# Optimization experiments

Hardware: AMD Instinct MI355X
Metric: run time of the kernel (lower is better)

Reference implementation:

```python
import jax, jax.numpy as jnp
import numpy as np

N_NODES, N_EDGES, NUM_GRAPHS = 50000, 800000, 64
F_DIM, H_DIM, N_LAYERS, N_CLASSES = 64, 64, 3, 16
EPS = 1e-5  # StdAggregation epsilon (PyG)


def setup_inputs() -> dict:
    key = jax.random.key(0)
    ks = jax.random.split(key, 12)
    s = 0.05
    x = jax.random.normal(ks[0], (N_NODES, F_DIM), jnp.float32)
    edge_index = jax.random.randint(ks[1], (2, N_EDGES), 0, N_NODES, dtype=jnp.int32)
    batch = jnp.sort(jax.random.randint(ks[2], (N_NODES,), 0, NUM_GRAPHS, dtype=jnp.int32))
    # per-layer PNAConv params (towers=1): pre Linear(2F->F), post Linear(13F->H), lin Linear(H->H)
    pre_w = jax.random.normal(ks[3], (N_LAYERS, F_DIM, 2 * F_DIM), jnp.float32) * s
    pre_b = jnp.zeros((N_LAYERS, F_DIM), jnp.float32)
    post_w = jax.random.normal(ks[4], (N_LAYERS, H_DIM, 13 * F_DIM), jnp.float32) * s
    post_b = jnp.zeros((N_LAYERS, H_DIM), jnp.float32)
    lin_w = jax.random.normal(ks[5], (N_LAYERS, H_DIM, H_DIM), jnp.float32) * s
    lin_b = jnp.zeros((N_LAYERS, H_DIM), jnp.float32)
    mlp_w1 = jax.random.normal(ks[6], (H_DIM, H_DIM), jnp.float32) * s
    mlp_b1 = jnp.zeros((H_DIM,), jnp.float32)
    mlp_w2 = jax.random.normal(ks[7], (N_CLASSES, H_DIM), jnp.float32) * s
    mlp_b2 = jnp.zeros((N_CLASSES,), jnp.float32)
    return dict(x=x, edge_index=edge_index, batch=batch,
                pre_w=pre_w, pre_b=pre_b, post_w=post_w, post_b=post_b,
                lin_w=lin_w, lin_b=lin_b, mlp_w1=mlp_w1, mlp_b1=mlp_b1,
                mlp_w2=mlp_w2, mlp_b2=mlp_b2)


def pna_forward(x, src, dst, pre_w, pre_b, post_w, post_b, lin_w, lin_b,
                mlp_w1, mlp_b1, mlp_w2, mlp_b2, batch):
    N = x.shape[0]
    deg_raw = jax.ops.segment_sum(jnp.ones_like(src, jnp.float32), dst, N)  # in-degree [N]
    deg = jnp.maximum(deg_raw, 1.0)[:, None]
    # avg log degree (PNA avg_deg['log'] from the degree histogram of this graph)
    avg_log = jnp.mean(jnp.log(deg_raw + 1.0))
    log_deg = jnp.log(deg + 1.0)
    amp = log_deg / avg_log          # amplification scaler [N,1]
    att = avg_log / log_deg          # attenuation scaler [N,1]
    has_in = (deg_raw > 0)[:, None]

    for l in range(pre_w.shape[0]):
        h = jnp.concatenate([x[dst], x[src]], axis=-1)        # [E, 2F] (x_i, x_j)
        m = h @ pre_w[l].T + pre_b[l]                          # pre_nn message [E, F]
        s1 = jax.ops.segment_sum(m, dst, N)
        s2 = jax.ops.segment_sum(m * m, dst, N)
        mean = s1 / deg
        std = jnp.sqrt(jax.nn.relu(s2 / deg - mean * mean) + EPS)
        mn = jnp.where(has_in, jax.ops.segment_min(m, dst, N), 0.0)
        mx = jnp.where(has_in, jax.ops.segment_max(m, dst, N), 0.0)
        aggr = jnp.concatenate([mean, mn, mx, std], axis=-1)   # [N, 4F]
        out = jnp.concatenate([x, aggr, aggr * amp, aggr * att], axis=-1)  # [N, 13F]
        out = out @ post_w[l].T + post_b[l]                    # post_nn [N, H]
        x = jax.nn.relu(out @ lin_w[l].T + lin_b[l])           # conv.lin + outer ReLU

    # global mean pool over graphs
    counts = jnp.maximum(
        jax.ops.segment_sum(jnp.ones((N,), x.dtype), batch, NUM_GRAPHS), 1.0)
    g = jax.ops.segment_sum(x, batch, NUM_GRAPHS) / counts[:, None]  # [G, H]
    g = jax.nn.relu(g @ mlp_w1.T + mlp_b1)
    return g @ mlp_w2.T + mlp_b2                               # [G, C]


def reference(x, edge_index, batch, pre_w, pre_b, post_w, post_b,
              lin_w, lin_b, mlp_w1, mlp_b1, mlp_w2, mlp_b2):
    src, dst = edge_index[0], edge_index[1]
    return pna_forward(x, src, dst, pre_w, pre_b, post_w, post_b,
                       lin_w, lin_b, mlp_w1, mlp_b1, mlp_w2, mlp_b2, batch)
```

## Files before the change

### kernel.cpp

```cpp
#include <hip/hip_runtime.h>
#include <math.h>

#define N_NODES   50000
#define N_EDGES   800000
#define NUM_GRAPHS 64
#define FDIM      64
#define HDIM      64
#define NLAYERS   3
#define NCLASSES  16
#define EPS       1e-5f

#define SCAN_CHUNK 1024
#define NCHUNKS ((N_NODES + SCAN_CHUNK - 1) / SCAN_CHUNK)

typedef unsigned short u16;
typedef unsigned int   u32;
typedef __attribute__((ext_vector_type(8))) short short8;
typedef __attribute__((ext_vector_type(4))) float floatx4;

#define WKS_LAYER 159744
#define PRES_LAYER 24576

__device__ inline void split1(float f, u16& h, u16& m, u16& l) {
    u32 b  = __float_as_uint(f);
    u32 hb = b & 0xFFFF0000u;
    float r = f - __uint_as_float(hb);
    u32 mb = __float_as_uint(r) & 0xFFFF0000u;
    float r2 = r - __uint_as_float(mb);
    u32 lb = __float_as_uint(r2) & 0xFFFF0000u;
    h = (u16)(hb >> 16); m = (u16)(mb >> 16); l = (u16)(lb >> 16);
}

__device__ inline void gl_lds16(const void* g, void* l) {
    __builtin_amdgcn_global_load_lds(
        (const __attribute__((address_space(1))) u32*)g,
        (__attribute__((address_space(3))) u32*)l, 16, 0, 0);
}

__global__ __launch_bounds__(256) void k_comb(const float* __restrict__ post_w,
                                              const float* __restrict__ lin_w,
                                              const float* __restrict__ pre_w,
                                              const float* __restrict__ post_b,
                                              const float* __restrict__ lin_b,
                                              u16* __restrict__ WkS,
                                              u16* __restrict__ PreS,
                                              float* __restrict__ bcv,
                                              int* __restrict__ cnt,
                                              float* __restrict__ logsum) {
    int b = blockIdx.x, t = threadIdx.x;
    int zi = b * 256 + t;
    if (zi < N_NODES) cnt[zi] = 0;
    if (zi == 0) *logsum = 0.f;

    if (b < 624) {
        int c  = t & 63;
        int kl = t >> 6;
        int l  = b / 208;
        int o  = (b % 208) * 4 + kl;
        const float* lw = lin_w + (size_t)l * 4096 + c * 64;
        const float* pw = post_w + (size_t)l * 53248 + o;
        float acc = 0.f;
        #pragma unroll 8
        for (int j = 0; j < 64; ++j)
            acc += lw[j] * pw[(size_t)j * 832];
        u16 h, m, lo;
        split1(acc, h, m, lo);

        int kn;
        if (o < 64) kn = o;
        else {
            int s  = (o - 64) >> 8;
            int mm = (o - 64) & 255;
            int j  = mm >> 5, r = mm & 31;
            kn = 64 + j * 96 + s * 32 + r;
        }
        int ch  = kn >> 5;
        int kin = kn & 31;
        int n16 = c & 15, nt = c >> 4;
        int swk = (((kin >> 3) + (n16 >> 1)) & 3) * 8 + (kin & 7);
        size_t base = (size_t)l * WKS_LAYER + (size_t)ch * 6144
                    + nt * 512 + n16 * 32 + swk;
        WkS[base]        = h;
        WkS[base + 2048] = m;
        WkS[base + 4096] = lo;
    } else if (b == 624) {
        if (t < 192) {
            int l = t >> 6, c = t & 63;
            float acc = lin_b[l * 64 + c];
            for (int j = 0; j < 64; ++j)
                acc += lin_w[(size_t)l * 4096 + c * 64 + j] * post_b[l * 64 + j];
            bcv[l * 64 + c] = acc;
        }
    } else {
        int i = (b - 625) * 256 + t;
        int l = i >> 13;
        int rem = i & 8191;
        int c128 = rem >> 6;
        int k = rem & 63;
        float v;
        if (c128 < 64) v = pre_w[(size_t)l * 8192 + c128 * 128 + k];
        else           v = pre_w[(size_t)l * 8192 + (c128 - 64) * 128 + 64 + k];
        u16 h, m, lo;
        split1(v, h, m, lo);
        int ch = k >> 5, kin = k & 31;
        int nt = c128 >> 4, n16 = c128 & 15;
        int swk = (((kin >> 3) + (n16 >> 1)) & 3) * 8 + (kin & 7);
        size_t base = (size_t)l * PRES_LAYER + (size_t)ch * 12288
                    + nt * 512 + n16 * 32 + swk;
        PreS[base]        = h;
        PreS[base + 4096] = m;
        PreS[base + 8192] = lo;
    }
}

__global__ void k_count(const int* __restrict__ dst, int* __restrict__ cnt,
                        int* __restrict__ rank) {
    int e = blockIdx.x * 256 + threadIdx.x;
    if (e < N_EDGES) rank[e] = atomicAdd(&cnt[dst[e]], 1);
}

__global__ void k_chunk_sums(const int* __restrict__ cnt, int* __restrict__ bsum,
                             float* __restrict__ logsum) {
    __shared__ int   ired[256];
    __shared__ float lred[256];
    int b = blockIdx.x, t = threadIdx.x;
    int base = b * SCAN_CHUNK;
    int s = 0; float ls = 0.f;
    for (int i = t; i < SCAN_CHUNK; i += 256) {
        int idx = base + i;
        if (idx < N_NODES) {
            int v = cnt[idx];
            s += v;
            ls += logf((float)v + 1.0f);
        }
    }
    ired[t] = s; lred[t] = ls;
    __syncthreads();
    for (int off = 128; off > 0; off >>= 1) {
        if (t < off) { ired[t] += ired[t + off]; lred[t] += lred[t + off]; }
        __syncthreads();
    }
    if (t == 0) { bsum[b] = ired[0]; atomicAdd(logsum, lred[0]); }
}

__global__ void k_scan_top(const int* __restrict__ bsum, int* __restrict__ boff,
                           int* __restrict__ row_start) {
    if (threadIdx.x == 0) {
        int acc = 0;
        for (int i = 0; i < NCHUNKS; ++i) { boff[i] = acc; acc += bsum[i]; }
        row_start[N_NODES] = acc;
    }
}

__global__ void k_scan_chunks(const int* __restrict__ cnt, const int* __restrict__ boff,
                              int* __restrict__ row_start) {
    __shared__ int tsum[256];
    int b = blockIdx.x, t = threadIdx.x;
    int base = b * SCAN_CHUNK + t * 4;
    int v[4]; int s = 0;
    #pragma unroll
    for (int i = 0; i < 4; ++i) {
        int idx = base + i;
        v[i] = (idx < N_NODES) ? cnt[idx] : 0;
        s += v[i];
    }
    tsum[t] = s;
    __syncthreads();
    for (int off = 1; off < 256; off <<= 1) {
        int val = (t >= off) ? tsum[t - off] : 0;
        __syncthreads();
        tsum[t] += val;
        __syncthreads();
    }
    int excl = boff[b] + tsum[t] - s;
    #pragma unroll
    for (int i = 0; i < 4; ++i) {
        int idx = base + i;
        if (idx < N_NODES) row_start[idx] = excl;
        excl += v[i];
    }
}

__global__ void k_scatter(const int* __restrict__ src, const int* __restrict__ dst,
                          const int* __restrict__ rank,
                          const int* __restrict__ row_start,
                          int* __restrict__ csr_src) {
    int e = blockIdx.x * 256 + threadIdx.x;
    if (e < N_EDGES) {
        int d = dst[e];
        csr_src[row_start[d] + rank[e]] = src[e];
    }
}

__global__ void k_scal(const int* __restrict__ cnt, const float* __restrict__ logsum,
                       float* __restrict__ inv_deg, float* __restrict__ ampv,
                       float* __restrict__ attv, float* __restrict__ g_sum,
                       int* __restrict__ g_cnt) {
    int n = blockIdx.x * 256 + threadIdx.x;
    if (blockIdx.x == 0) {
        for (int i = threadIdx.x; i < 4096; i += 256) g_sum[i] = 0.f;
        if (threadIdx.x < 64) g_cnt[threadIdx.x] = 0;
    }
    if (n < N_NODES) {
        float avg = logsum[0] / (float)N_NODES;
        float degf = fmaxf((float)cnt[n], 1.0f);
        inv_deg[n] = 1.0f / degf;
        float ld = logf(degf + 1.0f);
        ampv[n] = ld / avg;
        attv[n] = avg / ld;
    }
}

__global__ __launch_bounds__(256, 4) void k_pre(const float* __restrict__ x,
                                                const u16* __restrict__ PreS,
                                                const float* __restrict__ pre_b,
                                                float* __restrict__ p,
                                                float* __restrict__ q) {
    __shared__ u16 ldsB[2 * 12288];
    int t = threadIdx.x;
    int w = t >> 6;
    int lane = t & 63;
    int m = lane & 15;
    int qh = lane >> 4;
    int rowBase = blockIdx.x * 64;

    int myrow = rowBase + 16 * w + m;
    bool vr = myrow < N_NODES;
    int crow = vr ? myrow : 0;
    const float* xrow = x + (size_t)crow * 64;

    int bo = m * 32 + ((qh + (m >> 1)) & 3) * 8;

    #pragma unroll
    for (int ch = 0; ch < 2; ++ch) {
        const char* g = (const char*)PreS + (size_t)ch * 24576 + w * 6144 + lane * 16;
        char* l = (char*)ldsB + ch * 24576 + w * 6144;
        #pragma unroll
        for (int i = 0; i < 6; ++i)
            gl_lds16(g + i * 1024, l + i * 1024);
    }
    float fa[2][8];
    #pragma unroll
    for (int ch = 0; ch < 2; ++ch) {
        const float* sp = xrow + ch * 32 + qh * 8;
        float4 u0 = *(const float4*)sp;
        float4 u1 = *(const float4*)(sp + 4);
        fa[ch][0] = vr ? u0.x : 0.f; fa[ch][1] = vr ? u0.y : 0.f;
        fa[ch][2] = vr ? u0.z : 0.f; fa[ch][3] = vr ? u0.w : 0.f;
        fa[ch][4] = vr ? u1.x : 0.f; fa[ch][5] = vr ? u1.y : 0.f;
        fa[ch][6] = vr ? u1.z : 0.f; fa[ch][7] = vr ? u1.w : 0.f;
    }
    asm volatile("s_waitcnt vmcnt(0)" ::: "memory");
    __syncthreads();

    floatx4 acc[8] = {};
    #pragma unroll
    for (int ch = 0; ch < 2; ++ch) {
        union { u32 u[4]; short8 s8; } AH, AM, AL;
        #pragma unroll
        for (int i = 0; i < 4; ++i) {
            float f0 = fa[ch][2 * i], f1 = fa[ch][2 * i + 1];
            u32 b0 = __float_as_uint(f0), b1 = __float_as_uint(f1);
            u32 h0 = b0 & 0xFFFF0000u,  h1 = b1 & 0xFFFF0000u;
            float r0 = f0 - __uint_as_float(h0);
            float r1 = f1 - __uint_as_float(h1);
            u32 m0 = __float_as_uint(r0) & 0xFFFF0000u;
            u32 m1 = __float_as_uint(r1) & 0xFFFF0000u;
            float s0 = r0 - __uint_as_float(m0);
            float s1 = r1 - __uint_as_float(m1);
            u32 l0 = __float_as_uint(s0) & 0xFFFF0000u;
            u32 l1 = __float_as_uint(s1) & 0xFFFF0000u;
            AH.u[i] = (h0 >> 16) | h1;
            AM.u[i] = (m0 >> 16) | m1;
            AL.u[i] = (l0 >> 16) | l1;
        }
        const u16* Bb = ldsB + ch * 12288;
        #pragma unroll
        for (int nt = 0; nt < 8; ++nt) {
            short8 bH = *(const short8*)(Bb + nt * 512 + bo);
            short8 bM = *(const short8*)(Bb + 4096 + nt * 512 + bo);
            short8 bL = *(const short8*)(Bb + 8192 + nt * 512 + bo);
            acc[nt] = __builtin_amdgcn_mfma_f32_16x16x32_bf16(AH.s8, bH, acc[nt], 0, 0, 0);
            acc[nt] = __builtin_amdgcn_mfma_f32_16x16x32_bf16(AH.s8, bM, acc[nt], 0, 0, 0);
            acc[nt] = __builtin_amdgcn_mfma_f32_16x16x32_bf16(AM.s8, bH, acc[nt], 0, 0, 0);
            acc[nt] = __builtin_amdgcn_mfma_f32_16x16x32_bf16(AH.s8, bL, acc[nt], 0, 0, 0);
            acc[nt] = __builtin_amdgcn_mfma_f32_16x16x32_bf16(AM.s8, bM, acc[nt], 0, 0, 0);
            acc[nt] = __builtin_amdgcn_mfma_f32_16x16x32_bf16(AL.s8, bH, acc[nt], 0, 0, 0);
        }
    }

    int col = m;
    #pragma unroll
    for (int nt = 0; nt < 8; ++nt) {
        int cbase = (nt & 3) * 16 + col;
        float bias = (nt < 4) ? pre_b[cbase] : 0.f;
        float* outp = (nt < 4) ? p : q;
        #pragma unroll
        for (int reg = 0; reg < 4; ++reg) {
            int grow = rowBase + 16 * w + qh * 4 + reg;
            if (grow < N_NODES)
                outp[(size_t)grow * 64 + cbase] = acc[nt][reg] + bias;
        }
    }
}

__global__ __launch_bounds__(256) void k_aggr(const float* __restrict__ p,
                                              const float* __restrict__ q,
                                              const int* __restrict__ row_start,
                                              const int* __restrict__ csr_src,
                                              const float* __restrict__ inv_deg,
                                              float* __restrict__ aggr) {
    int wid  = (blockIdx.x * 256 + threadIdx.x) >> 6;
    int lane = threadIdx.x & 63;
    if (wid >= N_NODES) return;
    int n = wid;
    int beg = row_start[n], end = row_start[n + 1];
    float sum = 0.f, sq = 0.f;
    float mn = INFINITY, mx = -INFINITY;
    int e = beg;
    for (; e + 15 < end; e += 16) {
        int idx[16];
        #pragma unroll
        for (int u = 0; u < 16; ++u) idx[u] = csr_src[e + u];
        float qv[16];
        #pragma unroll
        for (int u = 0; u < 16; ++u) qv[u] = q[(size_t)idx[u] * 64 + lane];
        #pragma unroll
        for (int u = 0; u < 16; ++u) {
            float m = qv[u];
            sum += m; sq += m * m;
            mn = fminf(mn, m); mx = fmaxf(mx, m);
        }
    }
    for (; e + 7 < end; e += 8) {
        int idx[8];
        #pragma unroll
        for (int u = 0; u < 8; ++u) idx[u] = csr_src[e + u];
        float qv[8];
        #pragma unroll
        for (int u = 0; u < 8; ++u) qv[u] = q[(size_t)idx[u] * 64 + lane];
        #pragma unroll
        for (int u = 0; u < 8; ++u) {
            float m = qv[u];
            sum += m; sq += m * m;
            mn = fminf(mn, m); mx = fmaxf(mx, m);
        }
    }
    for (; e + 3 < end; e += 4) {
        int idx[4];
        #pragma unroll
        for (int u = 0; u < 4; ++u) idx[u] = csr_src[e + u];
        float qv[4];
        #pragma unroll
        for (int u = 0; u < 4; ++u) qv[u] = q[(size_t)idx[u] * 64 + lane];
        #pragma unroll
        for (int u = 0; u < 4; ++u) {
            float m = qv[u];
            sum += m; sq += m * m;
            mn = fminf(mn, m); mx = fmaxf(mx, m);
        }
    }
    for (; e < end; ++e) {
        int s = csr_src[e];
        float m = q[(size_t)s * 64 + lane];
        sum += m; sq += m * m;
        mn = fminf(mn, m); mx = fmaxf(mx, m);
    }
    float* a = aggr + (size_t)n * 256;
    if (end <= beg) {
        a[lane]       = 0.f;
        a[64 + lane]  = 0.f;
        a[128 + lane] = 0.f;
        a[192 + lane] = sqrtf(EPS);
    } else {
        float pv = p[n * 64 + lane];
        float id = inv_deg[n];
        float meanq = sum * id;
        float var = fmaxf(sq * id - meanq * meanq, 0.f);
        a[lane]       = pv + meanq;
        a[64 + lane]  = pv + mn;
        a[128 + lane] = pv + mx;
        a[192 + lane] = sqrtf(var + EPS);
    }
}

__global__ __launch_bounds__(256, 4) void k_post(const float* __restrict__ x,
                                                 const float* __restrict__ aggr,
                                                 const float* __restrict__ ampv,
                                                 const float* __restrict__ attv,
                                                 const u16* __restrict__ WkS,
                                                 const float* __restrict__ bc,
                                                 float* __restrict__ xout) {
    __shared__ u16 ldsB[3 * 6144];
    int t = threadIdx.x;
    int w = t >> 6;
    int lane = t & 63;
    int m = lane & 15;
    int qh = lane >> 4;
    int rowBase = blockIdx.x * 64;

    int myrow = rowBase + 16 * w + m;
    bool vr = myrow < N_NODES;
    int crow = vr ? myrow : 0;
    float ampR = vr ? ampv[crow] : 0.f;
    float attR = vr ? attv[crow] : 0.f;
    const float* xrow = x + (size_t)crow * 64;
    const float* arow = aggr + (size_t)crow * 256;

    int bo = m * 32 + ((qh + (m >> 1)) & 3) * 8;

    floatx4 acc[4] = {};
    float fc[8], fn[8];

    auto aptr = [&](int ch) -> const float* {
        if (ch <= 0) return xrow;
        if (ch == 1) return xrow + 32;
        int j = (ch - 2) / 3;
        if (j > 7) j = 7;
        return arow + j * 32;
    };
    auto loadRaw = [&](const float* sp, float* f) {
        float4 u0 = *(const float4*)(sp + qh * 8);
        float4 u1 = *(const float4*)(sp + qh * 8 + 4);
        f[0] = vr ? u0.x : 0.f; f[1] = vr ? u0.y : 0.f;
        f[2] = vr ? u0.z : 0.f; f[3] = vr ? u0.w : 0.f;
        f[4] = vr ? u1.x : 0.f; f[5] = vr ? u1.y : 0.f;
        f[6] = vr ? u1.z : 0.f; f[7] = vr ? u1.w : 0.f;
    };
    auto stageIssue = [&](int ch, int buf) {
        const char* g = (const char*)WkS + (size_t)ch * 12288 + w * 3072 + lane * 16;
        char* l = (char*)ldsB + buf * 12288 + w * 3072;
        #pragma unroll
        for (int i = 0; i < 3; ++i)
            gl_lds16(g + i * 1024, l + i * 1024);
    };

    loadRaw(aptr(0), fc);
    stageIssue(0, 0);
    stageIssue(1, 1);
    asm volatile("s_waitcnt vmcnt(3)" ::: "memory");
    asm volatile("s_barrier" ::: "memory");

    for (int ch = 0; ch < 26; ++ch) {
        loadRaw(aptr(ch + 1), fn);
        int ch2 = (ch + 2 < 26) ? ch + 2 : ch + 2 - 26;
        stageIssue(ch2, (ch + 2) % 3);

        float sc = 1.f;
        if (ch >= 2) {
            int s = (ch - 2) % 3;
            sc = (s == 0) ? 1.f : ((s == 1) ? ampR : attR);
        }

        union { u32 u[4]; short8 s8; } AH, AM, AL;
        #pragma unroll
        for (int i = 0; i < 4; ++i) {
            float f0 = fc[2 * i] * sc, f1 = fc[2 * i + 1] * sc;
            u32 b0 = __float_as_uint(f0), b1 = __float_as_uint(f1);
            u32 h0 = b0 & 0xFFFF0000u,  h1 = b1 & 0xFFFF0000u;
            float r0 = f0 - __uint_as_float(h0);
            float r1 = f1 - __uint_as_float(h1);
            u32 m0 = __float_as_uint(r0) & 0xFFFF0000u;
            u32 m1 = __float_as_uint(r1) & 0xFFFF0000u;
            float s0 = r0 - __uint_as_float(m0);
            float s1 = r1 - __uint_as_float(m1);
            u32 l0 = __float_as_uint(s0) & 0xFFFF0000u;
            u32 l1 = __float_as_uint(s1) & 0xFFFF0000u;
            AH.u[i] = (h0 >> 16) | h1;
            AM.u[i] = (m0 >> 16) | m1;
            AL.u[i] = (l0 >> 16) | l1;
        }

        const u16* Bb = ldsB + (ch % 3) * 6144;
        #pragma unroll
        for (int nt = 0; nt < 4; ++nt) {
            short8 bH = *(const short8*)(Bb + nt * 512 + bo);
            short8 bM = *(const short8*)(Bb + 2048 + nt * 512 + bo);
            short8 bL = *(const short8*)(Bb + 4096 + nt * 512 + bo);
            acc[nt] = __builtin_amdgcn_mfma_f32_16x16x32_bf16(AH.s8, bH, acc[nt], 0, 0, 0);
            acc[nt] = __builtin_amdgcn_mfma_f32_16x16x32_bf16(AH.s8, bM, acc[nt], 0, 0, 0);
            acc[nt] = __builtin_amdgcn_mfma_f32_16x16x32_bf16(AM.s8, bH, acc[nt], 0, 0, 0);
            acc[nt] = __builtin_amdgcn_mfma_f32_16x16x32_bf16(AH.s8, bL, acc[nt], 0, 0, 0);
            acc[nt] = __builtin_amdgcn_mfma_f32_16x16x32_bf16(AM.s8, bM, acc[nt], 0, 0, 0);
            acc[nt] = __builtin_amdgcn_mfma_f32_16x16x32_bf16(AL.s8, bH, acc[nt], 0, 0, 0);
        }

        asm volatile("s_waitcnt vmcnt(5)" ::: "memory");
        asm volatile("s_barrier" ::: "memory");

        #pragma unroll
        for (int i = 0; i < 8; ++i) fc[i] = fn[i];
    }

    int col = lane & 15;
    #pragma unroll
    for (int nt = 0; nt < 4; ++nt) {
        float bias = bc[nt * 16 + col];
        #pragma unroll
        for (int reg = 0; reg < 4; ++reg) {
            int grow = rowBase + 16 * w + qh * 4 + reg;
            if (grow < N_NODES) {
                xout[(size_t)grow * 64 + nt * 16 + col] =
                    fmaxf(acc[nt][reg] + bias, 0.f);
            }
        }
    }
}

__global__ __launch_bounds__(256) void k_pool(const float* __restrict__ x,
                                              const int* __restrict__ batch,
                                              float* __restrict__ g_sum,
                                              int* __restrict__ g_cnt) {
    int lane = threadIdx.x & 63;
    int wave = blockIdx.x * 4 + (threadIdx.x >> 6);
    const int NPW = 16;
    int beg = wave * NPW;
    if (beg >= N_NODES) return;
    int end = min(beg + NPW, N_NODES);
    float acc = 0.f;
    int cur = batch[beg];
    int c = 0;
    for (int n = beg; n < end; ++n) {
        int b = batch[n];
        if (b != cur) {
            atomicAdd(&g_sum[cur * 64 + lane], acc);
            if (lane == 0) atomicAdd(&g_cnt[cur], c);
            acc = 0.f; c = 0; cur = b;
        }
        acc += x[n * 64 + lane];
        ++c;
    }
    atomicAdd(&g_sum[cur * 64 + lane], acc);
    if (lane == 0) atomicAdd(&g_cnt[cur], c);
}

__global__ __launch_bounds__(256) void k_mlp(const float* __restrict__ g_sum,
                                             const int* __restrict__ g_cnt,
                                             const float* __restrict__ w1,
                                             const float* __restrict__ b1,
                                             const float* __restrict__ w2,
                                             const float* __restrict__ b2,
                                             float* __restrict__ out) {
    __shared__ float g[64][64];
    __shared__ float h[64][64];
    __shared__ float wT[64][65];
    int t = threadIdx.x;
    for (int idx = t; idx < 4096; idx += 256) {
        int gi = idx >> 6, c = idx & 63;
        float cntf = fmaxf((float)g_cnt[gi], 1.f);
        g[gi][c] = g_sum[idx] / cntf;
    }
    for (int idx = t; idx < 4096; idx += 256) {
        int c = idx >> 6, k = idx & 63;
        wT[k][c] = w1[c * 64 + k];
    }
    __syncthreads();
    for (int idx = t; idx < 4096; idx += 256) {
        int gi = idx >> 6, c = idx & 63;
        float acc = b1[c];
        for (int k = 0; k < 64; ++k) acc += g[gi][k] * wT[k][c];
        h[gi][c] = fmaxf(acc, 0.f);
    }
    __syncthreads();
    for (int idx = t; idx < 64 * NCLASSES; idx += 256) {
        int gi = idx >> 4, c = idx & 15;
        float acc = b2[c];
        for (int k = 0; k < 64; ++k) acc += h[gi][k] * w2[c * 64 + k];
        out[gi * NCLASSES + c] = acc;
    }
}

extern "C" void kernel_launch(void* const* d_in, const int* in_sizes, int n_in,
                              void* d_out, int out_size, void* d_ws, size_t ws_size,
                              hipStream_t stream) {
    const float* x      = (const float*)d_in[0];
    const int*   ei     = (const int*)d_in[1];
    const int*   batch  = (const int*)d_in[2];
    const float* pre_w  = (const float*)d_in[3];
    const float* pre_b  = (const float*)d_in[4];
    const float* post_w = (const float*)d_in[5];
    const float* post_b = (const float*)d_in[6];
    const float* lin_w  = (const float*)d_in[7];
    const float* lin_b  = (const float*)d_in[8];
    const float* mlp_w1 = (const float*)d_in[9];
    const float* mlp_b1 = (const float*)d_in[10];
    const float* mlp_w2 = (const float*)d_in[11];
    const float* mlp_b2 = (const float*)d_in[12];

    const int* src = ei;
    const int* dst = ei + N_EDGES;

    char* base = (char*)d_ws;
    size_t off = 0;
    auto alloc = [&](size_t bytes) -> void* {
        void* ptr = base + off;
        off += (bytes + 255) & ~(size_t)255;
        return ptr;
    };
    int*   cnt       = (int*)alloc(N_NODES * 4);
    int*   row_start = (int*)alloc((N_NODES + 1) * 4);
    int*   rank      = (int*)alloc(N_EDGES * 4);
    int*   csr_src   = (int*)alloc(N_EDGES * 4);
    int*   bsum      = (int*)alloc(64 * 4);
    int*   boff      = (int*)alloc(64 * 4);
    float* logsum    = (float*)alloc(16);
    float* inv_deg   = (float*)alloc(N_NODES * 4);
    float* ampv      = (float*)alloc(N_NODES * 4);
    float* attv      = (float*)alloc(N_NODES * 4);
    float* p         = (float*)alloc((size_t)N_NODES * 64 * 4);
    float* q         = (float*)alloc((size_t)N_NODES * 64 * 4);
    float* aggr      = (float*)alloc((size_t)N_NODES * 256 * 4);
    float* xb0       = (float*)alloc((size_t)N_NODES * 64 * 4);
    float* xb1       = (float*)alloc((size_t)N_NODES * 64 * 4);
    float* g_sum     = (float*)alloc(64 * 64 * 4);
    int*   g_cnt     = (int*)alloc(64 * 4);
    u16*   WkS       = (u16*)alloc((size_t)3 * WKS_LAYER * 2);
    u16*   PreS      = (u16*)alloc((size_t)3 * PRES_LAYER * 2);
    float* bcv       = (float*)alloc(3 * 64 * 4);

    k_comb<<<721, 256, 0, stream>>>(post_w, lin_w, pre_w, post_b, lin_b,
                                    WkS, PreS, bcv, cnt, logsum);

    k_count<<<(N_EDGES + 255) / 256, 256, 0, stream>>>(dst, cnt, rank);
    k_chunk_sums<<<NCHUNKS, 256, 0, stream>>>(cnt, bsum, logsum);
    k_scan_top<<<1, 64, 0, stream>>>(bsum, boff, row_start);
    k_scan_chunks<<<NCHUNKS, 256, 0, stream>>>(cnt, boff, row_start);
    k_scatter<<<(N_EDGES + 255) / 256, 256, 0, stream>>>(src, dst, rank,
                                                         row_start, csr_src);
    k_scal<<<(N_NODES + 255) / 256, 256, 0, stream>>>(cnt, logsum, inv_deg,
                                                      ampv, attv, g_sum, g_cnt);

    const int GEMM_BLOCKS = (N_NODES + 63) / 64;
    const float* xin = x;
    float* bufs[3] = {xb0, xb1, xb0};
    for (int l = 0; l < NLAYERS; ++l) {
        k_pre<<<GEMM_BLOCKS, 256, 0, stream>>>(xin, PreS + (size_t)l * PRES_LAYER,
                                               pre_b + l * 64, p, q);
        k_aggr<<<(N_NODES + 3) / 4, 256, 0, stream>>>(p, q, row_start, csr_src,
                                                      inv_deg, aggr);
        float* xo = bufs[l];
        k_post<<<GEMM_BLOCKS, 256, 0, stream>>>(xin, aggr, ampv, attv,
                                                WkS + (size_t)l * WKS_LAYER,
                                                bcv + l * 64, xo);
        xin = xo;
    }

    int pool_waves = (N_NODES + 15) / 16;
    k_pool<<<(pool_waves + 3) / 4, 256, 0, stream>>>(xin, batch, g_sum, g_cnt);
    k_mlp<<<1, 256, 0, stream>>>(g_sum, g_cnt, mlp_w1, mlp_b1, mlp_w2, mlp_b2,
                                 (float*)d_out);
}
```

Measured before the change: 480.8 us.

## Fuse next-layer pre GEMM into post kernel and merge scan kernels

The separate pre-projection kernel for layers 1 and 2 goes away: each post kernel now reloads the next layer's split-bf16 pre weights into LDS and computes p/q from the x rows it just wrote. The multi-kernel prefix scan, log-degree reduction and scalar kernel are merged into one single-block 1024-thread kernel. This removes several launches and one round trip of x through global memory per layer. The cost is a serial single-block scan over 50k nodes and longer, more register-hungry post blocks.

After: 666.7 us. +38.7%, slower.

```diff
diff --git a/kernel.cpp b/kernel.cpp
--- a/kernel.cpp
+++ b/kernel.cpp
@@ -10,9 +10,6 @@
 #define NCLASSES  16
 #define EPS       1e-5f
 
-#define SCAN_CHUNK 1024
-#define NCHUNKS ((N_NODES + SCAN_CHUNK - 1) / SCAN_CHUNK)
-
 typedef unsigned short u16;
 typedef unsigned int   u32;
 typedef __attribute__((ext_vector_type(8))) short short8;
@@ -45,12 +42,10 @@
                                               u16* __restrict__ WkS,
                                               u16* __restrict__ PreS,
                                               float* __restrict__ bcv,
-                                              int* __restrict__ cnt,
-                                              float* __restrict__ logsum) {
+                                              int* __restrict__ cnt) {
     int b = blockIdx.x, t = threadIdx.x;
     int zi = b * 256 + t;
     if (zi < N_NODES) cnt[zi] = 0;
-    if (zi == 0) *logsum = 0.f;
 
     if (b < 624) {
         int c  = t & 63;
@@ -119,65 +114,55 @@
     if (e < N_EDGES) rank[e] = atomicAdd(&cnt[dst[e]], 1);
 }
 
-__global__ void k_chunk_sums(const int* __restrict__ cnt, int* __restrict__ bsum,
-                             float* __restrict__ logsum) {
-    __shared__ int   ired[256];
-    __shared__ float lred[256];
-    int b = blockIdx.x, t = threadIdx.x;
-    int base = b * SCAN_CHUNK;
+__global__ __launch_bounds__(1024) void k_scan1(const int* __restrict__ cnt,
+                                                int* __restrict__ row_start,
+                                                float* __restrict__ inv_deg,
+                                                float* __restrict__ ampv,
+                                                float* __restrict__ attv,
+                                                float* __restrict__ g_sum,
+                                                int* __restrict__ g_cnt) {
+    __shared__ int   tsum[1024];
+    __shared__ float lred[1024];
+    int t = threadIdx.x;
+    const int CH = 49;
+    int base = t * CH;
+
     int s = 0; float ls = 0.f;
-    for (int i = t; i < SCAN_CHUNK; i += 256) {
+    for (int i = 0; i < CH; ++i) {
         int idx = base + i;
         if (idx < N_NODES) {
-            int v = cnt[idx];
-            s += v;
-            ls += logf((float)v + 1.0f);
-        }
-    }
-    ired[t] = s; lred[t] = ls;
+            int c = cnt[idx];
+            s += c;
+            ls += logf((float)c + 1.f);
+        }
+    }
+    tsum[t] = s; lred[t] = ls;
     __syncthreads();
-    for (int off = 128; off > 0; off >>= 1) {
-        if (t < off) { ired[t] += ired[t + off]; lred[t] += lred[t + off]; }
+    for (int off = 1; off < 1024; off <<= 1) {
+        int   iv = (t >= off) ? tsum[t - off] : 0;
+        float fv = (t >= off) ? lred[t - off] : 0.f;
         __syncthreads();
-    }
-    if (t == 0) { bsum[b] = ired[0]; atomicAdd(logsum, lred[0]); }
-}
-
-__global__ void k_scan_top(const int* __restrict__ bsum, int* __restrict__ boff,
-                           int* __restrict__ row_start) {
-    if (threadIdx.x == 0) {
-        int acc = 0;
-        for (int i = 0; i < NCHUNKS; ++i) { boff[i] = acc; acc += bsum[i]; }
-        row_start[N_NODES] = acc;
-    }
-}
-
-__global__ void k_scan_chunks(const int* __restrict__ cnt, const int* __restrict__ boff,
-                              int* __restrict__ row_start) {
-    __shared__ int tsum[256];
-    int b = blockIdx.x, t = threadIdx.x;
-    int base = b * SCAN_CHUNK + t * 4;
-    int v[4]; int s = 0;
-    #pragma unroll
-    for (int i = 0; i < 4; ++i) {
+        tsum[t] += iv; lred[t] += fv;
+        __syncthreads();
+    }
+    float avg = lred[1023] / (float)N_NODES;
+    if (t == 0) row_start[N_NODES] = tsum[1023];
+    for (int i = t; i < 4096; i += 1024) g_sum[i] = 0.f;
+    if (t < 64) g_cnt[t] = 0;
+
+    int excl = tsum[t] - s;
+    for (int i = 0; i < CH; ++i) {
         int idx = base + i;
-        v[i] = (idx < N_NODES) ? cnt[idx] : 0;
-        s += v[i];
-    }
-    tsum[t] = s;
-    __syncthreads();
-    for (int off = 1; off < 256; off <<= 1) {
-        int val = (t >= off) ? tsum[t - off] : 0;
-        __syncthreads();
-        tsum[t] += val;
-        __syncthreads();
-    }
-    int excl = boff[b] + tsum[t] - s;
-    #pragma unroll
-    for (int i = 0; i < 4; ++i) {
-        int idx = base + i;
-        if (idx < N_NODES) row_start[idx] = excl;
-        excl += v[i];
+        if (idx < N_NODES) {
+            int c = cnt[idx];
+            row_start[idx] = excl;
+            excl += c;
+            float degf = fmaxf((float)c, 1.f);
+            inv_deg[idx] = 1.f / degf;
+            float ld = logf(degf + 1.f);
+            ampv[idx] = ld / avg;
+            attv[idx] = avg / ld;
+        }
     }
 }
 
@@ -189,25 +174,6 @@
     if (e < N_EDGES) {
         int d = dst[e];
         csr_src[row_start[d] + rank[e]] = src[e];
-    }
-}
-
-__global__ void k_scal(const int* __restrict__ cnt, const float* __restrict__ logsum,
-                       float* __restrict__ inv_deg, float* __restrict__ ampv,
-                       float* __restrict__ attv, float* __restrict__ g_sum,
-                       int* __restrict__ g_cnt) {
-    int n = blockIdx.x * 256 + threadIdx.x;
-    if (blockIdx.x == 0) {
-        for (int i = threadIdx.x; i < 4096; i += 256) g_sum[i] = 0.f;
-        if (threadIdx.x < 64) g_cnt[threadIdx.x] = 0;
-    }
-    if (n < N_NODES) {
-        float avg = logsum[0] / (float)N_NODES;
-        float degf = fmaxf((float)cnt[n], 1.0f);
-        inv_deg[n] = 1.0f / degf;
-        float ld = logf(degf + 1.0f);
-        ampv[n] = ld / avg;
-        attv[n] = avg / ld;
     }
 }
 
@@ -390,8 +356,12 @@
                                                  const float* __restrict__ attv,
                                                  const u16* __restrict__ WkS,
                                                  const float* __restrict__ bc,
-                                                 float* __restrict__ xout) {
-    __shared__ u16 ldsB[3 * 6144];
+                                                 float* __restrict__ xout,
+                                                 const u16* __restrict__ PreSn,
+                                                 const float* __restrict__ pre_bn,
+                                                 float* __restrict__ pout,
+                                                 float* __restrict__ qout) {
+    __shared__ u16 ldsB[24576];
     int t = threadIdx.x;
     int w = t >> 6;
     int lane = t & 63;
@@ -502,6 +472,82 @@
             if (grow < N_NODES) {
                 xout[(size_t)grow * 64 + nt * 16 + col] =
                     fmaxf(acc[nt][reg] + bias, 0.f);
+            }
+        }
+    }
+
+    if (PreSn != nullptr) {
+        asm volatile("s_waitcnt vmcnt(0)" ::: "memory");
+        __syncthreads();
+
+        #pragma unroll
+        for (int ch = 0; ch < 2; ++ch) {
+            const char* g = (const char*)PreSn + (size_t)ch * 24576 + w * 6144 + lane * 16;
+            char* l = (char*)ldsB + ch * 24576 + w * 6144;
+            #pragma unroll
+            for (int i = 0; i < 6; ++i)
+                gl_lds16(g + i * 1024, l + i * 1024);
+        }
+        const float* nxrow = xout + (size_t)crow * 64;
+        float fa[2][8];
+        #pragma unroll
+        for (int ch = 0; ch < 2; ++ch) {
+            const float* sp = nxrow + ch * 32 + qh * 8;
+            float4 u0 = *(const float4*)sp;
+            float4 u1 = *(const float4*)(sp + 4);
+            fa[ch][0] = vr ? u0.x : 0.f; fa[ch][1] = vr ? u0.y : 0.f;
+            fa[ch][2] = vr ? u0.z : 0.f; fa[ch][3] = vr ? u0.w : 0.f;
+            fa[ch][4] = vr ? u1.x : 0.f; fa[ch][5] = vr ? u1.y : 0.f;
+            fa[ch][6] = vr ? u1.z : 0.f; fa[ch][7] = vr ? u1.w : 0.f;
+        }
+        asm volatile("s_waitcnt vmcnt(0)" ::: "memory");
+        __syncthreads();
+
+        floatx4 acc2[8] = {};
+        #pragma unroll
+        for (int ch = 0; ch < 2; ++ch) {
+            union { u32 u[4]; short8 s8; } AH, AM, AL;
+            #pragma unroll
+            for (int i = 0; i < 4; ++i) {
+                float f0 = fa[ch][2 * i], f1 = fa[ch][2 * i + 1];
+                u32 b0 = __float_as_uint(f0), b1 = __float_as_uint(f1);
+                u32 h0 = b0 & 0xFFFF0000u,  h1 = b1 & 0xFFFF0000u;
+                float r0 = f0 - __uint_as_float(h0);
+                float r1 = f1 - __uint_as_float(h1);
+                u32 m0 = __float_as_uint(r0) & 0xFFFF0000u;
+                u32 m1 = __float_as_uint(r1) & 0xFFFF0000u;
+                float s0 = r0 - __uint_as_float(m0);
+                float s1 = r1 - __uint_as_float(m1);
+                u32 l0 = __float_as_uint(s0) & 0xFFFF0000u;
+                u32 l1 = __float_as_uint(s1) & 0xFFFF0000u;
+                AH.u[i] = (h0 >> 16) | h1;
+                AM.u[i] = (m0 >> 16) | m1;
+                AL.u[i] = (l0 >> 16) | l1;
+            }
+            const u16* Bb = ldsB + ch * 12288;
+            #pragma unroll
+            for (int nt = 0; nt < 8; ++nt) {
+                short8 bH = *(const short8*)(Bb + nt * 512 + bo);
+                short8 bM = *(const short8*)(Bb + 4096 + nt * 512 + bo);
+                short8 bL = *(const short8*)(Bb + 8192 + nt * 512 + bo);
+                acc2[nt] = __builtin_amdgcn_mfma_f32_16x16x32_bf16(AH.s8, bH, acc2[nt], 0, 0, 0);
+                acc2[nt] = __builtin_amdgcn_mfma_f32_16x16x32_bf16(AH.s8, bM, acc2[nt], 0, 0, 0);
+                acc2[nt] = __builtin_amdgcn_mfma_f32_16x16x32_bf16(AM.s8, bH, acc2[nt], 0, 0, 0);
+                acc2[nt] = __builtin_amdgcn_mfma_f32_16x16x32_bf16(AH.s8, bL, acc2[nt], 0, 0, 0);
+                acc2[nt] = __builtin_amdgcn_mfma_f32_16x16x32_bf16(AM.s8, bM, acc2[nt], 0, 0, 0);
+                acc2[nt] = __builtin_amdgcn_mfma_f32_16x16x32_bf16(AL.s8, bH, acc2[nt], 0, 0, 0);
+            }
+        }
+        #pragma unroll
+        for (int nt = 0; nt < 8; ++nt) {
+            int cbase = (nt & 3) * 16 + col;
+            float bias = (nt < 4) ? pre_bn[cbase] : 0.f;
+            float* outp = (nt < 4) ? pout : qout;
+            #pragma unroll
+            for (int reg = 0; reg < 4; ++reg) {
+                int grow = rowBase + 16 * w + qh * 4 + reg;
+                if (grow < N_NODES)
+                    outp[(size_t)grow * 64 + cbase] = acc2[nt][reg] + bias;
             }
         }
     }
@@ -601,9 +647,6 @@
     int*   row_start = (int*)alloc((N_NODES + 1) * 4);
     int*   rank      = (int*)alloc(N_EDGES * 4);
     int*   csr_src   = (int*)alloc(N_EDGES * 4);
-    int*   bsum      = (int*)alloc(64 * 4);
-    int*   boff      = (int*)alloc(64 * 4);
-    float* logsum    = (float*)alloc(16);
     float* inv_deg   = (float*)alloc(N_NODES * 4);
     float* ampv      = (float*)alloc(N_NODES * 4);
     float* attv      = (float*)alloc(N_NODES * 4);
@@ -619,34 +662,38 @@
     float* bcv       = (float*)alloc(3 * 64 * 4);
 
     k_comb<<<721, 256, 0, stream>>>(post_w, lin_w, pre_w, post_b, lin_b,
-                                    WkS, PreS, bcv, cnt, logsum);
+                                    WkS, PreS, bcv, cnt);
 
     k_count<<<(N_EDGES + 255) / 256, 256, 0, stream>>>(dst, cnt, rank);
-    k_chunk_sums<<<NCHUNKS, 256, 0, stream>>>(cnt, bsum, logsum);
-    k_scan_top<<<1, 64, 0, stream>>>(bsum, boff, row_start);
-    k_scan_chunks<<<NCHUNKS, 256, 0, stream>>>(cnt, boff, row_start);
+    k_scan1<<<1, 1024, 0, stream>>>(cnt, row_start, inv_deg, ampv, attv,
+                                    g_sum, g_cnt);
     k_scatter<<<(N_EDGES + 255) / 256, 256, 0, stream>>>(src, dst, rank,
                                                          row_start, csr_src);
-    k_scal<<<(N_NODES + 255) / 256, 256, 0, stream>>>(cnt, logsum, inv_deg,
-                                                      ampv, attv, g_sum, g_cnt);
 
     const int GEMM_BLOCKS = (N_NODES + 63) / 64;
-    const float* xin = x;
-    float* bufs[3] = {xb0, xb1, xb0};
-    for (int l = 0; l < NLAYERS; ++l) {
-        k_pre<<<GEMM_BLOCKS, 256, 0, stream>>>(xin, PreS + (size_t)l * PRES_LAYER,
-                                               pre_b + l * 64, p, q);
-        k_aggr<<<(N_NODES + 3) / 4, 256, 0, stream>>>(p, q, row_start, csr_src,
-                                                      inv_deg, aggr);
-        float* xo = bufs[l];
-        k_post<<<GEMM_BLOCKS, 256, 0, stream>>>(xin, aggr, ampv, attv,
-                                                WkS + (size_t)l * WKS_LAYER,
-                                                bcv + l * 64, xo);
-        xin = xo;
-    }
+    k_pre<<<GEMM_BLOCKS, 256, 0, stream>>>(x, PreS, pre_b, p, q);
+    k_aggr<<<(N_NODES + 3) / 4, 256, 0, stream>>>(p, q, row_start, csr_src,
+                                                  inv_deg, aggr);
+    k_post<<<GEMM_BLOCKS, 256, 0, stream>>>(x, aggr, ampv, attv,
+                                            WkS, bcv, xb0,
+                                            PreS + (size_t)1 * PRES_LAYER,
+                                            pre_b + 64, p, q);
+    k_aggr<<<(N_NODES + 3) / 4, 256, 0, stream>>>(p, q, row_start, csr_src,
+                                                  inv_deg, aggr);
+    k_post<<<GEMM_BLOCKS, 256, 0, stream>>>(xb0, aggr, ampv, attv,
+                                            WkS + (size_t)1 * WKS_LAYER,
+                                            bcv + 64, xb1,
+                                            PreS + (size_t)2 * PRES_LAYER,
+                                            pre_b + 128, p, q);
+    k_aggr<<<(N_NODES + 3) / 4, 256, 0, stream>>>(p, q, row_start, csr_src,
+                                                  inv_deg, aggr);
+    k_post<<<GEMM_BLOCKS, 256, 0, stream>>>(xb1, aggr, ampv, attv,
+                                            WkS + (size_t)2 * WKS_LAYER,
+                                            bcv + 128, xb0,
+                                            nullptr, nullptr, nullptr, nullptr);
 
     int pool_waves = (N_NODES + 15) / 16;
-    k_pool<<<(pool_waves + 3) / 4, 256, 0, stream>>>(xin, batch, g_sum, g_cnt);
+    k_pool<<<(pool_waves + 3) / 4, 256, 0, stream>>>(xb0, batch, g_sum, g_cnt);
     k_mlp<<<1, 256, 0, stream>>>(g_sum, g_cnt, mlp_w1, mlp_b1, mlp_w2, mlp_b2,
                                  (float*)d_out);
 }
```
